# Kernel tuning notes

Hardware: AMD Instinct MI355X
Metric: run time of the kernel (lower is better)

The kernel has to match this reference:

```python
import jax, jax.numpy as jnp
import numpy as np

V, C, H, L, FC, OUT, WS = 512, 256, 4, 6, 1024, 192, 4
HD = C // H
B, T = 8, 1024


def setup_inputs() -> dict:
    key = jax.random.key(0)
    ks = jax.random.split(key, 24)
    d = {}
    d['emb'] = jax.random.normal(ks[0], (V, C), jnp.float32) * C ** -0.5
    d['Wq'] = jax.random.normal(ks[1], (L, C, C), jnp.float32) * 0.02
    d['Wk'] = jax.random.normal(ks[2], (L, C, C), jnp.float32) * 0.02
    d['Wv'] = jax.random.normal(ks[3], (L, C, C), jnp.float32) * 0.02
    d['Wo'] = jax.random.normal(ks[4], (L, C, C), jnp.float32) * 0.02
    d['bq'] = jnp.zeros((L, C), jnp.float32)
    d['bk'] = jnp.zeros((L, C), jnp.float32)
    d['bv'] = jnp.zeros((L, C), jnp.float32)
    d['bo'] = jnp.zeros((L, C), jnp.float32)
    d['rel_k'] = jax.random.normal(ks[5], (L, 2 * WS + 1, HD), jnp.float32) * HD ** -0.5
    d['rel_v'] = jax.random.normal(ks[6], (L, 2 * WS + 1, HD), jnp.float32) * HD ** -0.5
    d['ln1_g'] = jnp.ones((L, C), jnp.float32)
    d['ln1_b'] = jnp.zeros((L, C), jnp.float32)
    d['ln2_g'] = jnp.ones((L, C), jnp.float32)
    d['ln2_b'] = jnp.zeros((L, C), jnp.float32)
    d['ffn_w1'] = jax.random.normal(ks[7], (L, C, FC), jnp.float32) * 0.02
    d['ffn_b1'] = jnp.zeros((L, FC), jnp.float32)
    d['ffn_w2'] = jax.random.normal(ks[8], (L, FC, C), jnp.float32) * 0.02
    d['ffn_b2'] = jnp.zeros((L, C), jnp.float32)
    d['proj_w'] = jax.random.normal(ks[9], (2 * OUT, C), jnp.float32) * 0.02
    d['proj_b'] = jnp.zeros((2 * OUT,), jnp.float32)
    d['tokens'] = jax.random.randint(ks[10], (B, T), 0, V)
    d['x_lengths'] = jax.random.randint(ks[11], (B,), T // 2, T + 1)
    return d


def _rel_to_abs(x):
    # x: [B,H,L,2L-1] -> [B,H,L,L]
    b, h, l, _ = x.shape
    x = jnp.pad(x, ((0, 0), (0, 0), (0, 0), (0, 1)))
    x = x.reshape(b, h, l * 2 * l)
    x = jnp.pad(x, ((0, 0), (0, 0), (0, l - 1)))
    x = x.reshape(b, h, l + 1, 2 * l - 1)
    return x[:, :, :l, l - 1:]


def _abs_to_rel(x):
    # x: [B,H,L,L] -> [B,H,L,2L-1]
    b, h, l, _ = x.shape
    x = jnp.pad(x, ((0, 0), (0, 0), (0, 0), (0, l - 1)))
    x = x.reshape(b, h, l * (2 * l - 1))
    x = jnp.pad(x, ((0, 0), (0, 0), (l, 0)))
    x = x.reshape(b, h, l, 2 * l)
    return x[:, :, :, 1:]


def _layernorm(x, g, b):
    m = jnp.mean(x, -1, keepdims=True)
    v = jnp.var(x, -1, keepdims=True)
    return (x - m) * jax.lax.rsqrt(v + 1e-5) * g + b


def _pad_rel(emb, t):
    # [2*WS+1, HD] -> [2t-1, HD] (t > WS+1 here)
    p = t - (WS + 1)
    return jnp.pad(emb, ((p, p), (0, 0)))


def _forward(emb, Wq, Wk, Wv, Wo, bq, bk, bv, bo, rel_k, rel_v, ln1_g, ln1_b,
             ln2_g, ln2_b, ffn_w1, ffn_b1, ffn_w2, ffn_b2, proj_w, proj_b,
             tokens, x_lengths):
    b, t = tokens.shape
    x = emb[tokens] * jnp.sqrt(jnp.float32(C))          # [B,T,C]
    mask = (jnp.arange(t)[None, :] < x_lengths[:, None]).astype(x.dtype)  # [B,T]
    attn_mask = mask[:, None, None, :] * mask[:, None, :, None]           # [B,1,T,T]

    for i in range(L):
        q = (x @ Wq[i] + bq[i]).reshape(b, t, H, HD).transpose(0, 2, 1, 3)
        k = (x @ Wk[i] + bk[i]).reshape(b, t, H, HD).transpose(0, 2, 1, 3)
        v = (x @ Wv[i] + bv[i]).reshape(b, t, H, HD).transpose(0, 2, 1, 3)
        q = q * HD ** -0.5
        scores = jnp.einsum('bhqd,bhkd->bhqk', q, k)
        rk = _pad_rel(rel_k[i], t)                      # [2T-1,HD]
        scores = scores + _rel_to_abs(jnp.einsum('bhqd,md->bhqm', q, rk))
        scores = jnp.where(attn_mask > 0, scores, -1e4)
        p = jax.nn.softmax(scores, axis=-1)             # [B,H,T,T]
        o = jnp.einsum('bhqk,bhkd->bhqd', p, v)
        rv = _pad_rel(rel_v[i], t)
        o = o + jnp.einsum('bhqm,md->bhqd', _abs_to_rel(p), rv)
        o = o.transpose(0, 2, 1, 3).reshape(b, t, C) @ Wo[i] + bo[i]
        x = _layernorm(x + o, ln1_g[i], ln1_b[i])
        f = jax.nn.relu(x @ ffn_w1[i] + ffn_b1[i]) @ ffn_w2[i] + ffn_b2[i]
        x = _layernorm(x + f, ln2_g[i], ln2_b[i])
        x = x * mask[:, :, None]

    x_bct = x.transpose(0, 2, 1)                        # [B,C,T]
    stats = (jnp.einsum('oc,bct->bot', proj_w, x_bct) + proj_b[None, :, None])
    stats = stats * mask[:, None, :]
    m, logs = stats[:, :OUT], stats[:, OUT:]
    return x_bct, m, logs, mask[:, None, :]


def reference(emb, Wq, Wk, Wv, Wo, bq, bk, bv, bo, rel_k, rel_v, ln1_g, ln1_b,
              ln2_g, ln2_b, ffn_w1, ffn_b1, ffn_w2, ffn_b2, proj_w, proj_b,
              tokens, x_lengths):
    return _forward(emb, Wq, Wk, Wv, Wo, bq, bk, bv, bo, rel_k, rel_v, ln1_g,
                    ln1_b, ln2_g, ln2_b, ffn_w1, ffn_b1, ffn_w2, ffn_b2,
                    proj_w, proj_b, tokens, x_lengths)
```

## Files before the change

### kernel.cpp

```cpp
#include <hip/hip_runtime.h>

typedef unsigned short u16;
typedef __attribute__((ext_vector_type(8))) short bf16x8;
typedef __attribute__((ext_vector_type(4))) float f32x4;

#define CC   256
#define HH   4
#define HD   64
#define LL   6
#define FCD  1024
#define OUTD 192
#define WSZ  4
#define BB   8
#define TT   1024
#define BT   8192

#define OFF_XBCT 0
#define OFF_M    2097152
#define OFF_LOGS 3670016
#define OFF_MASK 5242880

#define WT_Q   0
#define WT_K   65536
#define WT_V   131072
#define WT_O   196608
#define WT_W1  262144
#define WT_W2  524288
#define WT_LAYER 786432
#define WT_TOTAL (6 * WT_LAYER)

__device__ __forceinline__ float bf2f(u16 u) {
  union { unsigned int i; float f; } v; v.i = ((unsigned int)u) << 16; return v.f;
}
__device__ __forceinline__ u16 f2bf(float f) {
  union { float f; unsigned int i; } v; v.f = f;
  unsigned int x = v.i;
  return (u16)((x + 0x7fffu + ((x >> 16) & 1u)) >> 16);
}
__device__ __forceinline__ void ldv4(const float* p, float* o) {
  float4 v = *reinterpret_cast<const float4*>(p);
  o[0] = v.x; o[1] = v.y; o[2] = v.z; o[3] = v.w;
}
__device__ __forceinline__ float ld_e(const float* p) { return *p; }
__device__ __forceinline__ float ld_e(const u16* p)   { return bf2f(*p); }
__device__ __forceinline__ void st_e(float* p, float v) { *p = v; }
__device__ __forceinline__ void st_e(u16* p, float v)   { *p = f2bf(v); }

__device__ __forceinline__ void gload16(const u16* g, u16* l) {
  __builtin_amdgcn_global_load_lds(
      (const __attribute__((address_space(1))) unsigned int*)g,
      (__attribute__((address_space(3))) unsigned int*)l, 16, 0, 0);
}

__device__ __forceinline__ void stage8(const float* p, u16* d) {
  float4 a = *reinterpret_cast<const float4*>(p);
  float4 b = *reinterpret_cast<const float4*>(p + 4);
  d[0] = f2bf(a.x); d[1] = f2bf(a.y); d[2] = f2bf(a.z); d[3] = f2bf(a.w);
  d[4] = f2bf(b.x); d[5] = f2bf(b.y); d[6] = f2bf(b.z); d[7] = f2bf(b.w);
}
__device__ __forceinline__ void stage8(const u16* p, u16* d) {
  ushort4 a = *reinterpret_cast<const ushort4*>(p);
  ushort4 b = *reinterpret_cast<const ushort4*>(p + 4);
  d[0] = a.x; d[1] = a.y; d[2] = a.z; d[3] = a.w;
  d[4] = b.x; d[5] = b.y; d[6] = b.z; d[7] = b.w;
}

__global__ __launch_bounds__(256) void tc_k(
    const float* __restrict__ W, u16* __restrict__ WT,
    int K, int N, int dstStride)
{
  __shared__ float tl[32][33];
  const int tid = threadIdx.x;
  const int lx = tid & 31;
  const int ly = tid >> 5;
  const int n0 = blockIdx.x << 5;
  const int k0 = blockIdx.y << 5;
  const int z  = blockIdx.z;
  const float* Ws = W + (size_t)z * K * N;
  u16* WTd = WT + (size_t)z * dstStride;
#pragma unroll
  for (int r = 0; r < 4; ++r)
    tl[ly + r * 8][lx] = Ws[(size_t)(k0 + ly + r * 8) * N + (n0 + lx)];
  __syncthreads();
#pragma unroll
  for (int r = 0; r < 4; ++r)
    WTd[(size_t)(n0 + ly + r * 8) * K + (k0 + lx)] = f2bf(tl[lx][ly + r * 8]);
}

__global__ __launch_bounds__(256) void embed_k(
    const float* __restrict__ emb, const int* __restrict__ tokens,
    float* __restrict__ X, u16* __restrict__ Xb)
{
  const int i = blockIdx.x * 256 + threadIdx.x;
  const int bt = i >> 6;
  const int c  = (i & 63) << 2;
  float4 e = *reinterpret_cast<const float4*>(emb + (size_t)tokens[bt] * CC + c);
  e.x *= 16.0f; e.y *= 16.0f; e.z *= 16.0f; e.w *= 16.0f;
  *reinterpret_cast<float4*>(X + (size_t)i * 4) = e;
  if (Xb)
    *reinterpret_cast<ushort4*>(Xb + (size_t)i * 4) =
        make_ushort4(f2bf(e.x), f2bf(e.y), f2bf(e.z), f2bf(e.w));
}

template <typename CT>
__global__ __launch_bounds__(256) void gemm_t_k(
    const u16* __restrict__ A, int lda, const u16* __restrict__ B, int ldb,
    const float* __restrict__ bias, CT* __restrict__ C, int ldc,
    int K, float ps, int relu, int accum)
{
  __shared__ __align__(16) u16 As[64 * 64];
  __shared__ __align__(16) u16 Bs[64 * 64];
  const int tid  = threadIdx.x;
  const int lane = tid & 63;
  const int wv   = tid >> 6;
  const int bm = blockIdx.y * 64;
  const int bn = blockIdx.x * 64;
  const int l15 = lane & 15;
  const int lq  = lane >> 4;
  const int sb0 = wv << 10;
  const int sb1 = sb0 + 512;
  const int r0  = (wv << 4) + (lane >> 3);
  const int r1  = r0 + 8;
  const int sc  = ((lane & 7) ^ (lane >> 3)) << 3;
  const int asw = (l15 & 7) << 3;

  f32x4 acc[4];
#pragma unroll
  for (int nt = 0; nt < 4; ++nt) acc[nt] = (f32x4){0.0f, 0.0f, 0.0f, 0.0f};

  for (int k0 = 0; k0 < K; k0 += 64) {
    gload16(A + (size_t)(bm + r0) * lda + (k0 + sc), As + sb0);
    gload16(A + (size_t)(bm + r1) * lda + (k0 + sc), As + sb1);
    gload16(B + (size_t)(bn + r0) * ldb + (k0 + sc), Bs + sb0);
    gload16(B + (size_t)(bn + r1) * ldb + (k0 + sc), Bs + sb1);
    __syncthreads();
#pragma unroll
    for (int s = 0; s < 2; ++s) {
      const int cbase = (s << 5) | (lq << 3);
      const bf16x8 af = *reinterpret_cast<const bf16x8*>(
          As + (((wv << 4) + l15) << 6) + (cbase ^ asw));
#pragma unroll
      for (int nt = 0; nt < 4; ++nt) {
        const bf16x8 bf = *reinterpret_cast<const bf16x8*>(
            Bs + (((nt << 4) + l15) << 6) + (cbase ^ asw));
        acc[nt] = __builtin_amdgcn_mfma_f32_16x16x32_bf16(af, bf, acc[nt], 0, 0, 0);
      }
    }
    __syncthreads();
  }

#pragma unroll
  for (int nt = 0; nt < 4; ++nt) {
#pragma unroll
    for (int r = 0; r < 4; ++r) {
      const int row = bm + (wv << 4) + (lq << 2) + r;
      const int col = bn + (nt << 4) + l15;
      float vv = acc[nt][r];
      if (bias) vv += bias[col];
      vv *= ps;
      if (relu) vv = fmaxf(vv, 0.0f);
      const size_t ci = (size_t)row * ldc + col;
      if (accum) vv += ld_e(C + ci);
      st_e(C + ci, vv);
    }
  }
}

__global__ __launch_bounds__(256) void gemm_ln_k(
    const u16* __restrict__ A, int lda, const u16* __restrict__ B, int ldb,
    const float* __restrict__ bias,
    float* __restrict__ X, u16* __restrict__ Xb,
    const float* __restrict__ g, const float* __restrict__ be,
    const int* __restrict__ xlen, int am, int K)
{
  __shared__ __align__(16) u16 As[16 * 64];
  __shared__ __align__(16) u16 Bs[256 * 64];
  __shared__ float part[16][4];
  __shared__ float part2[16][4];
  const int tid  = threadIdx.x;
  const int lane = tid & 63;
  const int wv   = tid >> 6;
  const int bm   = blockIdx.x << 4;
  const int l15  = lane & 15;
  const int lq   = lane >> 4;
  const int sc   = ((lane & 7) ^ (lane >> 3)) << 3;
  const int asw  = (l15 & 7) << 3;

  f32x4 acc[4];
#pragma unroll
  for (int nt = 0; nt < 4; ++nt) acc[nt] = (f32x4){0.0f, 0.0f, 0.0f, 0.0f};

  for (int k0 = 0; k0 < K; k0 += 64) {
    if (wv < 2)
      gload16(A + (size_t)(bm + (wv << 3) + (lane >> 3)) * lda + (k0 + sc),
              As + (wv << 9));
#pragma unroll
    for (int j = 0; j < 8; ++j)
      gload16(B + (size_t)((wv << 6) + (j << 3) + (lane >> 3)) * ldb + (k0 + sc),
              Bs + (wv << 12) + (j << 9));
    __syncthreads();
#pragma unroll
    for (int s = 0; s < 2; ++s) {
      const int cbase = (s << 5) | (lq << 3);
      const bf16x8 af = *reinterpret_cast<const bf16x8*>(
          As + (l15 << 6) + (cbase ^ asw));
#pragma unroll
      for (int nt = 0; nt < 4; ++nt) {
        const bf16x8 bf = *reinterpret_cast<const bf16x8*>(
            Bs + (((wv << 6) + (nt << 4) + l15) << 6) + (cbase ^ asw));
        acc[nt] = __builtin_amdgcn_mfma_f32_16x16x32_bf16(af, bf, acc[nt], 0, 0, 0);
      }
    }
    __syncthreads();
  }

  float v[4][4];
#pragma unroll
  for (int nt = 0; nt < 4; ++nt) {
    const int col = (wv << 6) + (nt << 4) + l15;
#pragma unroll
    for (int reg = 0; reg < 4; ++reg) {
      const int gr = bm + (lq << 2) + reg;
      v[nt][reg] = acc[nt][reg] + bias[col] + X[(size_t)gr * CC + col];
    }
  }
  float sr[4];
#pragma unroll
  for (int reg = 0; reg < 4; ++reg) {
    float s = v[0][reg] + v[1][reg] + v[2][reg] + v[3][reg];
    s += __shfl_xor(s, 1); s += __shfl_xor(s, 2);
    s += __shfl_xor(s, 4); s += __shfl_xor(s, 8);
    sr[reg] = s;
  }
  if (l15 == 0) {
#pragma unroll
    for (int reg = 0; reg < 4; ++reg) part[(lq << 2) + reg][wv] = sr[reg];
  }
  __syncthreads();
  float mean[4];
#pragma unroll
  for (int reg = 0; reg < 4; ++reg) {
    const int r = (lq << 2) + reg;
    mean[reg] = (part[r][0] + part[r][1] + part[r][2] + part[r][3]) * (1.0f / CC);
  }
#pragma unroll
  for (int reg = 0; reg < 4; ++reg) {
    float s2 = 0.0f;
#pragma unroll
    for (int nt = 0; nt < 4; ++nt) {
      v[nt][reg] -= mean[reg];
      s2 += v[nt][reg] * v[nt][reg];
    }
    s2 += __shfl_xor(s2, 1); s2 += __shfl_xor(s2, 2);
    s2 += __shfl_xor(s2, 4); s2 += __shfl_xor(s2, 8);
    sr[reg] = s2;
  }
  if (l15 == 0) {
#pragma unroll
    for (int reg = 0; reg < 4; ++reg) part2[(lq << 2) + reg][wv] = sr[reg];
  }
  __syncthreads();
#pragma unroll
  for (int reg = 0; reg < 4; ++reg) {
    const int r = (lq << 2) + reg;
    const int gr = bm + r;
    const int b = gr >> 10;
    const int t = gr & (TT - 1);
    const float var = (part2[r][0] + part2[r][1] + part2[r][2] + part2[r][3]) * (1.0f / CC);
    const float rs = rsqrtf(var + 1e-5f);
    const bool zero = (am && t >= xlen[b]);
#pragma unroll
    for (int nt = 0; nt < 4; ++nt) {
      const int col = (wv << 6) + (nt << 4) + l15;
      float y = v[nt][reg] * rs * g[col] + be[col];
      if (zero) y = 0.0f;
      X[(size_t)gr * CC + col] = y;
      Xb[(size_t)gr * CC + col] = f2bf(y);
    }
  }
}

__global__ __launch_bounds__(256) void gemm_qkv_k(
    const u16* __restrict__ Xb, const u16* __restrict__ WTl,
    const float* __restrict__ bq, const float* __restrict__ bk,
    const float* __restrict__ bv,
    u16* __restrict__ Qb, u16* __restrict__ Kb, u16* __restrict__ Vb)
{
  __shared__ __align__(16) u16 pool[2 * 64 * 64];
  u16* As = pool;
  u16* Bs = pool + 4096;
  const int tid  = threadIdx.x;
  const int lane = tid & 63;
  const int wv   = tid >> 6;
  const int bx = blockIdx.x;
  const int bm = blockIdx.y * 64;
  const int mi = bx >> 2;
  const int bnl = (bx & 3) << 6;
  const int bng = bx << 6;
  const int l15 = lane & 15;
  const int lq  = lane >> 4;
  const int sb0 = wv << 10;
  const int sb1 = sb0 + 512;
  const int r0  = (wv << 4) + (lane >> 3);
  const int r1  = r0 + 8;
  const int sc  = ((lane & 7) ^ (lane >> 3)) << 3;
  const int asw = (l15 & 7) << 3;

  const float* bias = (mi == 0) ? bq : (mi == 1) ? bk : bv;
  const float ps = (mi == 0) ? 0.125f : 1.0f;

  f32x4 acc[4];
#pragma unroll
  for (int nt = 0; nt < 4; ++nt) acc[nt] = (f32x4){0.0f, 0.0f, 0.0f, 0.0f};

  for (int k0 = 0; k0 < CC; k0 += 64) {
    gload16(Xb  + (size_t)(bm + r0) * CC + (k0 + sc), As + sb0);
    gload16(Xb  + (size_t)(bm + r1) * CC + (k0 + sc), As + sb1);
    gload16(WTl + (size_t)(bng + r0) * CC + (k0 + sc), Bs + sb0);
    gload16(WTl + (size_t)(bng + r1) * CC + (k0 + sc), Bs + sb1);
    __syncthreads();
#pragma unroll
    for (int s = 0; s < 2; ++s) {
      const int cbase = (s << 5) | (lq << 3);
      const bf16x8 af = *reinterpret_cast<const bf16x8*>(
          As + (((wv << 4) + l15) << 6) + (cbase ^ asw));
#pragma unroll
      for (int nt = 0; nt < 4; ++nt) {
        const bf16x8 bf = *reinterpret_cast<const bf16x8*>(
            Bs + (((nt << 4) + l15) << 6) + (cbase ^ asw));
        acc[nt] = __builtin_amdgcn_mfma_f32_16x16x32_bf16(af, bf, acc[nt], 0, 0, 0);
      }
    }
    __syncthreads();
  }

  if (mi != 2) {
    u16* Cp = (mi == 0) ? Qb : Kb;
#pragma unroll
    for (int nt = 0; nt < 4; ++nt) {
#pragma unroll
      for (int r = 0; r < 4; ++r) {
        const int row = bm + (wv << 4) + (lq << 2) + r;
        const int col = bnl + (nt << 4) + l15;
        Cp[(size_t)row * CC + col] = f2bf((acc[nt][r] + bias[col]) * ps);
      }
    }
  } else {
    u16* Ts = pool;
#pragma unroll
    for (int nt = 0; nt < 4; ++nt) {
#pragma unroll
      for (int r = 0; r < 4; ++r) {
        const int tl = (wv << 4) + (lq << 2) + r;
        const int dl = (nt << 4) + l15;
        Ts[dl * 72 + tl] = f2bf(acc[nt][r] + bias[bnl + dl]);
      }
    }
    __syncthreads();
    const int dl = tid >> 2;
    const size_t rowbase =
        ((size_t)((bm >> 10) * 256 + bnl + dl) << 10) + (bm & (TT - 1));
#pragma unroll
    for (int j = 0; j < 4; ++j) {
      const int c4 = ((tid & 3) << 2) + (j << 4);
      *reinterpret_cast<ushort4*>(Vb + rowbase + c4) =
          *reinterpret_cast<const ushort4*>(Ts + dl * 72 + c4);
    }
  }
}

template <typename AT, typename CT>
__global__ __launch_bounds__(256) void gemm_m_k(
    const AT* __restrict__ A, const float* __restrict__ W, int ldb,
    const float* __restrict__ bias, CT* __restrict__ C, int ldc,
    int K, float ps, int relu, int accum, int vtrans)
{
  __shared__ u16 As[64][40];
  __shared__ u16 Bs[64][40];
  const int tid  = threadIdx.x;
  const int lane = tid & 63;
  const int wv   = tid >> 6;
  const int bm = blockIdx.y * 64;
  const int bn = blockIdx.x * 64;
  const int l15 = lane & 15;
  const int lq  = lane >> 4;
  const int ar = tid >> 2;
  const int ak = (tid & 3) << 3;
  const int kr = tid & 31;
  const int nb = (tid >> 5) << 3;

  f32x4 acc[4];
#pragma unroll
  for (int nt = 0; nt < 4; ++nt) acc[nt] = (f32x4){0.0f, 0.0f, 0.0f, 0.0f};

  for (int k0 = 0; k0 < K; k0 += 32) {
    u16 t8[8];
    stage8(A + (size_t)(bm + ar) * K + (k0 + ak), t8);
    *reinterpret_cast<ushort4*>(&As[ar][ak]) =
        make_ushort4(t8[0], t8[1], t8[2], t8[3]);
    *reinterpret_cast<ushort4*>(&As[ar][ak + 4]) =
        make_ushort4(t8[4], t8[5], t8[6], t8[7]);
    float w8[8];
    ldv4(W + (size_t)(k0 + kr) * ldb + (bn + nb), w8);
    ldv4(W + (size_t)(k0 + kr) * ldb + (bn + nb + 4), w8 + 4);
#pragma unroll
    for (int j = 0; j < 8; ++j) Bs[nb + j][kr] = f2bf(w8[j]);
    __syncthreads();

    const bf16x8 af = *reinterpret_cast<const bf16x8*>(&As[(wv << 4) + l15][lq << 3]);
#pragma unroll
    for (int nt = 0; nt < 4; ++nt) {
      const bf16x8 bf = *reinterpret_cast<const bf16x8*>(&Bs[(nt << 4) + l15][lq << 3]);
      acc[nt] = __builtin_amdgcn_mfma_f32_16x16x32_bf16(af, bf, acc[nt], 0, 0, 0);
    }
    __syncthreads();
  }

#pragma unroll
  for (int nt = 0; nt < 4; ++nt) {
#pragma unroll
    for (int r = 0; r < 4; ++r) {
      const int row = bm + (wv << 4) + (lq << 2) + r;
      const int col = bn + (nt << 4) + l15;
      float vv = acc[nt][r];
      if (bias) vv += bias[col];
      vv *= ps;
      if (relu) vv = fmaxf(vv, 0.0f);
      if (vtrans) {
        const size_t dst = ((size_t)((row >> 10) * 256 + col) << 10) + (row & (TT - 1));
        st_e(C + dst, vv);
      } else {
        const size_t ci = (size_t)row * ldc + col;
        if (accum) vv += ld_e(C + ci);
        st_e(C + ci, vv);
      }
    }
  }
}

#define KLp(g) (KVpool + (g) * 4096)
#define VTp(g) (KVpool + 8192 + (g) * 4096)
__global__ __launch_bounds__(512, 4) void fattn_k(
    const u16* __restrict__ Qb, const u16* __restrict__ Kb,
    const u16* __restrict__ VbT, const float* __restrict__ rk,
    const float* __restrict__ rv, const int* __restrict__ xlen,
    u16* __restrict__ Ob)
{
  __shared__ __align__(16) u16 KVpool[4 * 64 * 64];
  __shared__ u16  Pl[2][64][64];
  __shared__ float rkl[9][64];
  __shared__ float rvl[9][68];
  __shared__ float qrel[64][12];
  __shared__ float bs_s[64][12];
  __shared__ float mrow_s[64];

  const int qt = blockIdx.x;
  const int bh = blockIdx.y;
  const int b  = bh >> 2;
  const int h  = bh & 3;
  const int tid  = threadIdx.x;
  const int lane = tid & 63;
  const int wv   = tid >> 6;
  const int grp  = wv >> 2;
  const int wvl  = wv & 3;
  const int gtid = tid & 255;
  const int l15  = lane & 15;
  const int lq   = lane >> 4;
  const int len = xlen[b];
  const int q0  = qt << 6;
  const int m0  = wvl << 4;

  if (q0 >= len) {
    for (int i = tid; i < 64 * 16; i += 512) {
      const int r = i >> 4, c4 = (i & 15) << 2;
      *reinterpret_cast<ushort4*>(
          Ob + (size_t)((b << 10) + q0 + r) * CC + (h << 6) + c4) =
          make_ushort4(0, 0, 0, 0);
    }
    return;
  }

  for (int i = tid; i < 9 * 64; i += 512) {
    rkl[i >> 6][i & 63] = rk[i];
    rvl[i >> 6][i & 63] = rv[i];
  }
  for (int i = tid; i < 64 * 16; i += 512) {
    const int r = i >> 4, c4 = (i & 15) << 2;
    *reinterpret_cast<ushort4*>(&Pl[0][r][c4]) = *reinterpret_cast<const ushort4*>(
        Qb + (size_t)((b << 10) + q0 + r) * CC + (h << 6) + c4);
  }
  for (int i = tid; i < 64 * 12; i += 512) (&bs_s[0][0])[i] = -3.0e38f;
  __syncthreads();
  for (int i = tid; i < 64 * 9; i += 512) {
    const int r = i / 9, j = i - r * 9;
    float s = 0.0f;
#pragma unroll 16
    for (int d = 0; d < 64; ++d) s += bf2f(Pl[0][r][d]) * rkl[j][d];
    qrel[r][j] = s;
  }
  __syncthreads();

  const bf16x8 qa0 = *reinterpret_cast<const bf16x8*>(&Pl[0][m0 + l15][lq << 3]);
  const bf16x8 qa1 = *reinterpret_cast<const bf16x8*>(&Pl[0][m0 + l15][32 + (lq << 3)]);

  f32x4 oacc[4];
#pragma unroll
  for (int nt = 0; nt < 4; ++nt) oacc[nt] = (f32x4){0.0f, 0.0f, 0.0f, 0.0f};
  float m_r[4] = {-3.0e38f, -3.0e38f, -3.0e38f, -3.0e38f};
  float l_r[4] = {0.0f, 0.0f, 0.0f, 0.0f};

  const int gr = gtid >> 2;
  const int gc = (gtid & 3) << 4;
  const int rswG = (gr & 7) << 3;
  const int c0w = gc ^ rswG;
  const int c1w = (gc + 8) ^ rswG;
  const int rswF = (l15 & 7) << 3;

  const int nkt = (len + 63) >> 6;
  const int nt0 = (nkt + 1) >> 1;
  const int myBeg = grp ? nt0 : 0;
  const int myEnd = grp ? nkt : nt0;

  u16* klp = KLp(grp);
  u16* vtp = VTp(grp);
  u16* plp = &Pl[grp][0][0];

  bf16x8 kp0, kp1, vq0, vq1;
  if (myBeg < myEnd) {
    const int k0 = myBeg << 6;
    const u16* p = Kb + (size_t)((b << 10) + k0 + gr) * CC + (h << 6) + gc;
    kp0 = *reinterpret_cast<const bf16x8*>(p);
    kp1 = *reinterpret_cast<const bf16x8*>(p + 8);
    const u16* pv = VbT + (size_t)((bh << 6) + gr) * TT + k0 + gc;
    vq0 = *reinterpret_cast<const bf16x8*>(pv);
    vq1 = *reinterpret_cast<const bf16x8*>(pv + 8);
  }

  for (int it = 0; it < nt0; ++it) {
    const int kt = myBeg + it;
    const bool act = (kt < myEnd);
    if (act) {
      *reinterpret_cast<bf16x8*>(klp + gr * 64 + c0w) = kp0;
      *reinterpret_cast<bf16x8*>(klp + gr * 64 + c1w) = kp1;
      *reinterpret_cast<bf16x8*>(vtp + gr * 64 + c0w) = vq0;
      *reinterpret_cast<bf16x8*>(vtp + gr * 64 + c1w) = vq1;
    }
    __syncthreads();

    if (act && kt + 1 < myEnd) {
      const int kn = (kt + 1) << 6;
      const u16* p = Kb + (size_t)((b << 10) + kn + gr) * CC + (h << 6) + gc;
      kp0 = *reinterpret_cast<const bf16x8*>(p);
      kp1 = *reinterpret_cast<const bf16x8*>(p + 8);
      const u16* pv = VbT + (size_t)((bh << 6) + gr) * TT + kn + gc;
      vq0 = *reinterpret_cast<const bf16x8*>(pv);
      vq1 = *reinterpret_cast<const bf16x8*>(pv + 8);
    }

    if (act) {
      const int k0 = kt << 6;
      f32x4 sacc[4];
#pragma unroll
      for (int nt = 0; nt < 4; ++nt) sacc[nt] = (f32x4){0.0f, 0.0f, 0.0f, 0.0f};
#pragma unroll
      for (int nt = 0; nt < 4; ++nt) {
        const int row = (nt << 4) + l15;
        const bf16x8 b0 = *reinterpret_cast<const bf16x8*>(klp + row * 64 + ((lq << 3) ^ rswF));
        const bf16x8 b1 = *reinterpret_cast<const bf16x8*>(klp + row * 64 + ((32 + (lq << 3)) ^ rswF));
        sacc[nt] = __builtin_amdgcn_mfma_f32_16x16x32_bf16(qa0, b0, sacc[nt], 0, 0, 0);
        sacc[nt] = __builtin_amdgcn_mfma_f32_16x16x32_bf16(qa1, b1, sacc[nt], 0, 0, 0);
      }
#pragma unroll
      for (int nt = 0; nt < 4; ++nt) {
#pragma unroll
        for (int reg = 0; reg < 4; ++reg) {
          const int m = m0 + (lq << 2) + reg;
          const int q = q0 + m;
          const int k = k0 + (nt << 4) + l15;
          float s = sacc[nt][reg];
          const int r = k - q;
          const bool band = (r >= -WSZ && r <= WSZ);
          if (band) s += qrel[m][r + WSZ];
          if (q >= len || k >= len) s = -10000.0f;
          if (band) bs_s[m][r + WSZ] = s;
          sacc[nt][reg] = s;
        }
      }
      float aa[4];
#pragma unroll
      for (int reg = 0; reg < 4; ++reg) {
        float mx = fmaxf(fmaxf(sacc[0][reg], sacc[1][reg]),
                         fmaxf(sacc[2][reg], sacc[3][reg]));
        mx = fmaxf(mx, __shfl_xor(mx, 1));
        mx = fmaxf(mx, __shfl_xor(mx, 2));
        mx = fmaxf(mx, __shfl_xor(mx, 4));
        mx = fmaxf(mx, __shfl_xor(mx, 8));
        const float mo = m_r[reg];
        const float mn = fmaxf(mo, mx);
        const float a = __expf(mo - mn);
        m_r[reg] = mn; aa[reg] = a; l_r[reg] *= a;
      }
#pragma unroll
      for (int reg = 0; reg < 4; ++reg) {
        const int m = m0 + (lq << 2) + reg;
        const int msw = (m & 7) << 3;
        const float mn = m_r[reg];
        float ssum = 0.0f;
#pragma unroll
        for (int nt = 0; nt < 4; ++nt) {
          const float p = __expf(sacc[nt][reg] - mn);
          ssum += p;
          plp[m * 64 + (((nt << 4) + l15) ^ msw)] = f2bf(p);
        }
        ssum += __shfl_xor(ssum, 1);
        ssum += __shfl_xor(ssum, 2);
        ssum += __shfl_xor(ssum, 4);
        ssum += __shfl_xor(ssum, 8);
        l_r[reg] += ssum;
      }
#pragma unroll
      for (int nt = 0; nt < 4; ++nt) {
#pragma unroll
        for (int reg = 0; reg < 4; ++reg) oacc[nt][reg] *= aa[reg];
      }
      {
        const int prow = m0 + l15;
        const bf16x8 p0 = *reinterpret_cast<const bf16x8*>(plp + prow * 64 + ((lq << 3) ^ rswF));
        const bf16x8 p1 = *reinterpret_cast<const bf16x8*>(plp + prow * 64 + ((32 + (lq << 3)) ^ rswF));
#pragma unroll
        for (int nt = 0; nt < 4; ++nt) {
          const int row = (nt << 4) + l15;
          const bf16x8 v0 = *reinterpret_cast<const bf16x8*>(vtp + row * 64 + ((lq << 3) ^ rswF));
          const bf16x8 v1 = *reinterpret_cast<const bf16x8*>(vtp + row * 64 + ((32 + (lq << 3)) ^ rswF));
          oacc[nt] = __builtin_amdgcn_mfma_f32_16x16x32_bf16(p0, v0, oacc[nt], 0, 0, 0);
          oacc[nt] = __builtin_amdgcn_mfma_f32_16x16x32_bf16(p1, v1, oacc[nt], 0, 0, 0);
        }
      }
    }
    __syncthreads();
  }

  float* Oc = (float*)KVpool;
  float* mxp = Oc + 64 * 68;
  float* lxp = mxp + 64;
  if (grp == 1) {
#pragma unroll
    for (int nt = 0; nt < 4; ++nt)
#pragma unroll
      for (int reg = 0; reg < 4; ++reg)
        Oc[(m0 + (lq << 2) + reg) * 68 + (nt << 4) + l15] = oacc[nt][reg];
    if (l15 == 0) {
#pragma unroll
      for (int reg = 0; reg < 4; ++reg) {
        mxp[m0 + (lq << 2) + reg] = m_r[reg];
        lxp[m0 + (lq << 2) + reg] = l_r[reg];
      }
    }
  }
  __syncthreads();
  if (grp == 0) {
    float a0c[4], a1c[4];
#pragma unroll
    for (int reg = 0; reg < 4; ++reg) {
      const int m = m0 + (lq << 2) + reg;
      const float m1 = mxp[m], l1 = lxp[m];
      const float mo = m_r[reg];
      const float mn = fmaxf(mo, m1);
      const float a0 = __expf(mo - mn);
      const float a1 = __expf(m1 - mn);
      m_r[reg] = mn;
      l_r[reg] = a0 * l_r[reg] + a1 * l1;
      a0c[reg] = a0; a1c[reg] = a1;
    }
#pragma unroll
    for (int nt = 0; nt < 4; ++nt)
#pragma unroll
      for (int reg = 0; reg < 4; ++reg) {
        const int m = m0 + (lq << 2) + reg;
        oacc[nt][reg] = a0c[reg] * oacc[nt][reg]
                      + a1c[reg] * Oc[m * 68 + (nt << 4) + l15];
      }
    if (l15 == 0) {
#pragma unroll
      for (int reg = 0; reg < 4; ++reg)
        mrow_s[m0 + (lq << 2) + reg] = m_r[reg];
    }
  }
  __syncthreads();
  for (int i = tid; i < 64 * 9; i += 512) {
    const int r = i / 9, j = i - r * 9;
    qrel[r][j] = __expf(bs_s[r][j] - mrow_s[r]);
  }
  __syncthreads();
  if (grp == 0) {
#pragma unroll
    for (int nt = 0; nt < 4; ++nt) {
#pragma unroll
      for (int reg = 0; reg < 4; ++reg) {
        const int m = m0 + (lq << 2) + reg;
        float o = oacc[nt][reg];
#pragma unroll
        for (int j = 0; j < 9; ++j) o += qrel[m][j] * rvl[j][(nt << 4) + l15];
        o *= 1.0f / l_r[reg];
        Ob[(size_t)((b << 10) + q0 + m) * CC + (h << 6) + (nt << 4) + l15] = f2bf(o);
      }
    }
  }
}

__global__ __launch_bounds__(256) void addln_k(
    float* __restrict__ X, u16* __restrict__ Xb, const float* __restrict__ R,
    const float* __restrict__ g, const float* __restrict__ be,
    const int* __restrict__ xlen, int am)
{
  const int tid = threadIdx.x;
  const int row = blockIdx.x * 4 + (tid >> 6);
  const int lane = tid & 63;
  const int b = row >> 10;
  const int t = row & (TT - 1);
  const size_t base = (size_t)row * CC + lane * 4;
  float4 xv = *reinterpret_cast<const float4*>(X + base);
  float4 rv = *reinterpret_cast<const float4*>(R + base);
  float v0 = xv.x + rv.x, v1 = xv.y + rv.y, v2 = xv.z + rv.z, v3 = xv.w + rv.w;
  float s = v0 + v1 + v2 + v3;
#pragma unroll
  for (int off = 32; off > 0; off >>= 1) s += __shfl_xor(s, off);
  const float mean = s * (1.0f / CC);
  const float d0 = v0 - mean, d1 = v1 - mean, d2 = v2 - mean, d3 = v3 - mean;
  float s2 = d0 * d0 + d1 * d1 + d2 * d2 + d3 * d3;
#pragma unroll
  for (int off = 32; off > 0; off >>= 1) s2 += __shfl_xor(s2, off);
  const float rs = rsqrtf(s2 * (1.0f / CC) + 1e-5f);
  const float4 gv = *reinterpret_cast<const float4*>(g + lane * 4);
  const float4 bv = *reinterpret_cast<const float4*>(be + lane * 4);
  float y0 = d0 * rs * gv.x + bv.x;
  float y1 = d1 * rs * gv.y + bv.y;
  float y2 = d2 * rs * gv.z + bv.z;
  float y3 = d3 * rs * gv.w + bv.w;
  if (am && t >= xlen[b]) { y0 = 0.0f; y1 = 0.0f; y2 = 0.0f; y3 = 0.0f; }
  *reinterpret_cast<float4*>(X + base) = make_float4(y0, y1, y2, y3);
  if (Xb)
    *reinterpret_cast<ushort4*>(Xb + base) =
        make_ushort4(f2bf(y0), f2bf(y1), f2bf(y2), f2bf(y3));
}

__global__ __launch_bounds__(256) void proj_k(
    const float* __restrict__ A, const float* __restrict__ W,
    const float* __restrict__ bias, const int* __restrict__ xlen,
    float* __restrict__ out)
{
  __shared__ u16 As[64][40];
  __shared__ u16 Bs[64][40];
  const int tid  = threadIdx.x;
  const int lane = tid & 63;
  const int wv   = tid >> 6;
  const int bm = blockIdx.y * 64;
  const int bn = blockIdx.x * 64;
  const int l15 = lane & 15;
  const int lq  = lane >> 4;
  const int ar = tid >> 2;
  const int ak = (tid & 3) << 3;

  f32x4 acc[4];
#pragma unroll
  for (int nt = 0; nt < 4; ++nt) acc[nt] = (f32x4){0.0f, 0.0f, 0.0f, 0.0f};

  for (int k0 = 0; k0 < CC; k0 += 32) {
    u16 t8[8];
    stage8(A + (size_t)(bm + ar) * CC + (k0 + ak), t8);
    *reinterpret_cast<ushort4*>(&As[ar][ak]) =
        make_ushort4(t8[0], t8[1], t8[2], t8[3]);
    *reinterpret_cast<ushort4*>(&As[ar][ak + 4]) =
        make_ushort4(t8[4], t8[5], t8[6], t8[7]);
    stage8(W + (size_t)(bn + ar) * CC + (k0 + ak), t8);
    *reinterpret_cast<ushort4*>(&Bs[ar][ak]) =
        make_ushort4(t8[0], t8[1], t8[2], t8[3]);
    *reinterpret_cast<ushort4*>(&Bs[ar][ak + 4]) =
        make_ushort4(t8[4], t8[5], t8[6], t8[7]);
    __syncthreads();

    const bf16x8 af = *reinterpret_cast<const bf16x8*>(&As[(wv << 4) + l15][lq << 3]);
#pragma unroll
    for (int nt = 0; nt < 4; ++nt) {
      const bf16x8 bf = *reinterpret_cast<const bf16x8*>(&Bs[(nt << 4) + l15][lq << 3]);
      acc[nt] = __builtin_amdgcn_mfma_f32_16x16x32_bf16(af, bf, acc[nt], 0, 0, 0);
    }
    __syncthreads();
  }

#pragma unroll
  for (int nt = 0; nt < 4; ++nt) {
#pragma unroll
    for (int r = 0; r < 4; ++r) {
      const int row = bm + (wv << 4) + (lq << 2) + r;
      const int bb = row >> 10;
      const int t  = row & (TT - 1);
      const int len = xlen[bb];
      const int o = bn + (nt << 4) + l15;
      float vv = acc[nt][r] + bias[o];
      if (t >= len) vv = 0.0f;
      const size_t dst = (o < OUTD)
          ? (size_t)OFF_M    + ((size_t)bb * OUTD + o) * TT + t
          : (size_t)OFF_LOGS + ((size_t)bb * OUTD + (o - OUTD)) * TT + t;
      out[dst] = vv;
    }
  }
}

__global__ __launch_bounds__(256) void pack_xbct_k(
    const float* __restrict__ X, float* __restrict__ out)
{
  __shared__ float tl[32][33];
  const int tid = threadIdx.x;
  const int lx = tid & 31;
  const int ly = tid >> 5;
  const int c0 = blockIdx.x << 5;
  const int t0 = blockIdx.y << 5;
  const int b  = blockIdx.z;
#pragma unroll
  for (int r = 0; r < 4; ++r)
    tl[ly + r * 8][lx] = X[(((size_t)(b << 10) + t0 + ly + r * 8) << 8) + c0 + lx];
  __syncthreads();
#pragma unroll
  for (int r = 0; r < 4; ++r)
    out[OFF_XBCT + (((size_t)b * 256 + c0 + ly + r * 8) << 10) + t0 + lx] =
        tl[lx][ly + r * 8];
}

__global__ __launch_bounds__(256) void pack_mask_k(
    const int* __restrict__ xlen, float* __restrict__ out)
{
  const int i = blockIdx.x * 256 + threadIdx.x;
  const int b = i >> 10;
  const int t = i & (TT - 1);
  out[OFF_MASK + i] = (t < xlen[b]) ? 1.0f : 0.0f;
}

extern "C" void kernel_launch(void* const* d_in, const int* in_sizes, int n_in,
                              void* d_out, int out_size, void* d_ws, size_t ws_size,
                              hipStream_t stream)
{
  (void)in_sizes; (void)n_in; (void)out_size;
  const float* emb   = (const float*)d_in[0];
  const float* Wq    = (const float*)d_in[1];
  const float* Wk    = (const float*)d_in[2];
  const float* Wv    = (const float*)d_in[3];
  const float* Wo    = (const float*)d_in[4];
  const float* bq    = (const float*)d_in[5];
  const float* bk    = (const float*)d_in[6];
  const float* bv    = (const float*)d_in[7];
  const float* bo    = (const float*)d_in[8];
  const float* relk  = (const float*)d_in[9];
  const float* relv  = (const float*)d_in[10];
  const float* ln1g  = (const float*)d_in[11];
  const float* ln1b  = (const float*)d_in[12];
  const float* ln2g  = (const float*)d_in[13];
  const float* ln2b  = (const float*)d_in[14];
  const float* W1    = (const float*)d_in[15];
  const float* b1    = (const float*)d_in[16];
  const float* W2    = (const float*)d_in[17];
  const float* b2    = (const float*)d_in[18];
  const float* projw = (const float*)d_in[19];
  const float* projb = (const float*)d_in[20];
  const int*   tokens = (const int*)d_in[21];
  const int*   xlen   = (const int*)d_in[22];
  float* out = (float*)d_out;

  const size_t TIER_B_WS = 26214400ull;
  const size_t TIER_A_WS = 38797312ull;
  const int tier = (ws_size >= TIER_A_WS) ? 0 : (ws_size >= TIER_B_WS) ? 1 : 2;

  float* X  = (float*)d_ws;
  u16* ObU = (u16*)(out + OFF_XBCT);
  u16* Kb  = (u16*)(out + OFF_M);
  u16* Vb  = (u16*)(out + OFF_LOGS);
  float* T5 = out + OFF_M;

  if (tier <= 1) {
    u16* Xb  = (u16*)(X + (size_t)BT * CC);
    u16* Wbf = Xb + (size_t)BT * CC;
    u16* pool = Wbf + WT_TOTAL;
    u16* Qb = pool;
    u16* Hc = pool;
    const int CH = (tier == 0) ? 1 : 4;
    const int Wn = FCD / CH;

    tc_k<<<dim3(8, 8, 6), 256, 0, stream>>>(Wq, Wbf + WT_Q, CC, CC, WT_LAYER);
    tc_k<<<dim3(8, 8, 6), 256, 0, stream>>>(Wk, Wbf + WT_K, CC, CC, WT_LAYER);
    tc_k<<<dim3(8, 8, 6), 256, 0, stream>>>(Wv, Wbf + WT_V, CC, CC, WT_LAYER);
    tc_k<<<dim3(8, 8, 6), 256, 0, stream>>>(Wo, Wbf + WT_O, CC, CC, WT_LAYER);
    tc_k<<<dim3(32, 8, 6), 256, 0, stream>>>(W1, Wbf + WT_W1, CC, FCD, WT_LAYER);
    tc_k<<<dim3(8, 32, 6), 256, 0, stream>>>(W2, Wbf + WT_W2, FCD, CC, WT_LAYER);

    embed_k<<<(BT * CC / 4) / 256, 256, 0, stream>>>(emb, tokens, X, Xb);

    const dim3 gQKV(12, BT / 64);
    const dim3 gA(16, BB * HH);
    const dim3 gP((2 * OUTD) / 64, BT / 64);

    for (int l = 0; l < LL; ++l) {
      const u16* WTl = Wbf + (size_t)l * WT_LAYER;
      gemm_qkv_k<<<gQKV, 256, 0, stream>>>(Xb, WTl, bq + (size_t)l * CC,
                                           bk + (size_t)l * CC, bv + (size_t)l * CC,
                                           Qb, Kb, Vb);
      fattn_k<<<gA, 512, 0, stream>>>(Qb, Kb, Vb,
                                      relk + (size_t)l * (2 * WSZ + 1) * HD,
                                      relv + (size_t)l * (2 * WSZ + 1) * HD, xlen, ObU);
      gemm_ln_k<<<BT / 16, 256, 0, stream>>>(ObU, CC, WTl + WT_O, CC,
                                             bo + (size_t)l * CC, X, Xb,
                                             ln1g + (size_t)l * CC,
                                             ln1b + (size_t)l * CC, xlen, 0, CC);
      if (CH == 1) {
        gemm_t_k<u16><<<dim3(FCD / 64, BT / 64), 256, 0, stream>>>(
            Xb, CC, WTl + WT_W1, CC, b1 + (size_t)l * FCD, Hc, FCD, CC,
            1.0f, 1, 0);
        gemm_ln_k<<<BT / 16, 256, 0, stream>>>(Hc, FCD, WTl + WT_W2, FCD,
                                               b2 + (size_t)l * CC, X, Xb,
                                               ln2g + (size_t)l * CC,
                                               ln2b + (size_t)l * CC, xlen, 1, FCD);
      } else {
        const dim3 gC(CC / 64, BT / 64);
        for (int c = 0; c < CH; ++c) {
          gemm_t_k<u16><<<dim3(Wn / 64, BT / 64), 256, 0, stream>>>(
              Xb, CC, WTl + WT_W1 + (size_t)c * Wn * CC, CC,
              b1 + (size_t)l * FCD + c * Wn, Hc, Wn, CC, 1.0f, 1, 0);
          gemm_t_k<float><<<gC, 256, 0, stream>>>(
              Hc, Wn, WTl + WT_W2 + (size_t)c * Wn, FCD,
              (c == 0) ? (b2 + (size_t)l * CC) : nullptr, T5, CC, Wn,
              1.0f, 0, (c > 0));
        }
        addln_k<<<BT / 4, 256, 0, stream>>>(X, Xb, T5, ln2g + (size_t)l * CC,
                                            ln2b + (size_t)l * CC, xlen, 1);
      }
    }

    proj_k<<<gP, 256, 0, stream>>>(X, projw, projb, xlen, out);
  } else {
    u16* pool = (u16*)(X + (size_t)BT * CC);
    u16* Qb = pool;
    u16* Hc = pool;

    embed_k<<<(BT * CC / 4) / 256, 256, 0, stream>>>(emb, tokens, X, nullptr);

    const dim3 gC(CC / 64, BT / 64);
    const dim3 gA(16, BB * HH);
    const dim3 gP((2 * OUTD) / 64, BT / 64);

    for (int l = 0; l < LL; ++l) {
      const float* Wq_l = Wq + (size_t)l * CC * CC;
      const float* Wk_l = Wk + (size_t)l * CC * CC;
      const float* Wv_l = Wv + (size_t)l * CC * CC;
      const float* Wo_l = Wo + (size_t)l * CC * CC;

      gemm_m_k<float, u16><<<gC, 256, 0, stream>>>(X, Wq_l, CC, bq + (size_t)l * CC,
                                                   Qb, CC, CC, 0.125f, 0, 0, 0);
      gemm_m_k<float, u16><<<gC, 256, 0, stream>>>(X, Wk_l, CC, bk + (size_t)l * CC,
                                                   Kb, CC, CC, 1.0f, 0, 0, 0);
      gemm_m_k<float, u16><<<gC, 256, 0, stream>>>(X, Wv_l, CC, bv + (size_t)l * CC,
                                                   Vb, CC, CC, 1.0f, 0, 0, 1);
      fattn_k<<<gA, 512, 0, stream>>>(Qb, Kb, Vb,
                                      relk + (size_t)l * (2 * WSZ + 1) * HD,
                                      relv + (size_t)l * (2 * WSZ + 1) * HD, xlen, ObU);
      gemm_m_k<u16, float><<<gC, 256, 0, stream>>>(ObU, Wo_l, CC, bo + (size_t)l * CC,
                                                   T5, CC, CC, 1.0f, 0, 0, 0);
      addln_k<<<BT / 4, 256, 0, stream>>>(X, nullptr, T5, ln1g + (size_t)l * CC,
                                          ln1b + (size_t)l * CC, xlen, 0);
      for (int c = 0; c < 4; ++c) {
        gemm_m_k<float, u16><<<gC, 256, 0, stream>>>(X, W1 + (size_t)l * CC * FCD + c * 256,
                                                     FCD, b1 + (size_t)l * FCD + c * 256,
                                                     Hc, 256, CC, 1.0f, 1, 0, 0);
        gemm_m_k<u16, float><<<gC, 256, 0, stream>>>(Hc,
                                                     W2 + (size_t)l * FCD * CC + (size_t)c * 256 * CC,
                                                     CC, (c == 0) ? (b2 + (size_t)l * CC) : nullptr,
                                                     T5, CC, 256, 1.0f, 0, (c > 0), 0);
      }
      addln_k<<<BT / 4, 256, 0, stream>>>(X, nullptr, T5, ln2g + (size_t)l * CC,
                                          ln2b + (size_t)l * CC, xlen, 1);
    }

    proj_k<<<gP, 256, 0, stream>>>(X, projw, projb, xlen, out);
  }

  pack_xbct_k<<<dim3(CC / 32, TT / 32, BB), 256, 0, stream>>>(X, out);
  pack_mask_k<<<(BB * TT) / 256, 256, 0, stream>>>(xlen, out);
}
```

Baseline: 692.6 us.

## Use 128x128-tile GEMM for FFN up-projection and raise MFMA priority in attention

Adds a gemm128_k kernel in which each wave computes a 64x64 sub-tile (4x4 MFMA fragments) of a 128x128 block, and uses it for the FFN W1 GEMM with ReLU in place of the 64x64-tile gemm_t_k. The larger tile reuses each A and B fragment loaded from LDS across more MFMAs, cutting LDS and global traffic per flop. The trade is more registers and only 512 blocks for the GEMM. It also wraps the MFMA sequences in the attention kernel with s_setprio(1)/s_setprio(0) so waves issuing matrix work are favored by the scheduler. gemm_ln_k is moved below gemm128_k unchanged, and the unused stage16 helper is added.

```diff
diff --git a/kernel.cpp b/kernel.cpp
--- a/kernel.cpp
+++ b/kernel.cpp
@@ -63,6 +63,10 @@
   ushort4 b = *reinterpret_cast<const ushort4*>(p + 4);
   d[0] = a.x; d[1] = a.y; d[2] = a.z; d[3] = a.w;
   d[4] = b.x; d[5] = b.y; d[6] = b.z; d[7] = b.w;
+}
+__device__ __forceinline__ void stage16(const u16* src, u16* dst) {
+  *reinterpret_cast<bf16x8*>(dst)     = *reinterpret_cast<const bf16x8*>(src);
+  *reinterpret_cast<bf16x8*>(dst + 8) = *reinterpret_cast<const bf16x8*>(src + 8);
 }
 
 __global__ __launch_bounds__(256) void tc_k(
@@ -166,116 +170,77 @@
   }
 }
 
-__global__ __launch_bounds__(256) void gemm_ln_k(
+template <typename CT>
+__global__ __launch_bounds__(256) void gemm128_k(
     const u16* __restrict__ A, int lda, const u16* __restrict__ B, int ldb,
-    const float* __restrict__ bias,
-    float* __restrict__ X, u16* __restrict__ Xb,
-    const float* __restrict__ g, const float* __restrict__ be,
-    const int* __restrict__ xlen, int am, int K)
-{
-  __shared__ __align__(16) u16 As[16 * 64];
-  __shared__ __align__(16) u16 Bs[256 * 64];
-  __shared__ float part[16][4];
-  __shared__ float part2[16][4];
+    const float* __restrict__ bias, CT* __restrict__ C, int ldc,
+    int K, float ps, int relu)
+{
+  __shared__ __align__(16) u16 As[128 * 64];
+  __shared__ __align__(16) u16 Bs[128 * 64];
   const int tid  = threadIdx.x;
   const int lane = tid & 63;
   const int wv   = tid >> 6;
-  const int bm   = blockIdx.x << 4;
-  const int l15  = lane & 15;
-  const int lq   = lane >> 4;
-  const int sc   = ((lane & 7) ^ (lane >> 3)) << 3;
-  const int asw  = (l15 & 7) << 3;
-
-  f32x4 acc[4];
-#pragma unroll
-  for (int nt = 0; nt < 4; ++nt) acc[nt] = (f32x4){0.0f, 0.0f, 0.0f, 0.0f};
+  const int bm = blockIdx.y * 128;
+  const int bn = blockIdx.x * 128;
+  const int l15 = lane & 15;
+  const int lq  = lane >> 4;
+  const int wr  = (wv >> 1) << 6;
+  const int wc  = (wv & 1) << 6;
+  const int rbase = wv << 5;
+  const int rlane = lane >> 3;
+  const int sc  = ((lane & 7) ^ rlane) << 3;
+  const int asw = (l15 & 7) << 3;
+
+  f32x4 acc[4][4];
+#pragma unroll
+  for (int mf = 0; mf < 4; ++mf)
+#pragma unroll
+    for (int nf = 0; nf < 4; ++nf) acc[mf][nf] = (f32x4){0.0f, 0.0f, 0.0f, 0.0f};
 
   for (int k0 = 0; k0 < K; k0 += 64) {
-    if (wv < 2)
-      gload16(A + (size_t)(bm + (wv << 3) + (lane >> 3)) * lda + (k0 + sc),
-              As + (wv << 9));
-#pragma unroll
-    for (int j = 0; j < 8; ++j)
-      gload16(B + (size_t)((wv << 6) + (j << 3) + (lane >> 3)) * ldb + (k0 + sc),
-              Bs + (wv << 12) + (j << 9));
+#pragma unroll
+    for (int j = 0; j < 4; ++j) {
+      gload16(A + (size_t)(bm + rbase + (j << 3) + rlane) * lda + (k0 + sc),
+              As + ((rbase + (j << 3)) << 6));
+      gload16(B + (size_t)(bn + rbase + (j << 3) + rlane) * ldb + (k0 + sc),
+              Bs + ((rbase + (j << 3)) << 6));
+    }
     __syncthreads();
 #pragma unroll
     for (int s = 0; s < 2; ++s) {
-      const int cbase = (s << 5) | (lq << 3);
-      const bf16x8 af = *reinterpret_cast<const bf16x8*>(
-          As + (l15 << 6) + (cbase ^ asw));
-#pragma unroll
-      for (int nt = 0; nt < 4; ++nt) {
+      const int cb = ((s << 5) | (lq << 3)) ^ asw;
+      bf16x8 af[4];
+#pragma unroll
+      for (int mf = 0; mf < 4; ++mf)
+        af[mf] = *reinterpret_cast<const bf16x8*>(
+            As + ((wr + (mf << 4) + l15) << 6) + cb);
+#pragma unroll
+      for (int nf = 0; nf < 4; ++nf) {
         const bf16x8 bf = *reinterpret_cast<const bf16x8*>(
-            Bs + (((wv << 6) + (nt << 4) + l15) << 6) + (cbase ^ asw));
-        acc[nt] = __builtin_amdgcn_mfma_f32_16x16x32_bf16(af, bf, acc[nt], 0, 0, 0);
-      }
-    }
-    __syncthreads();
-  }
-
-  float v[4][4];
-#pragma unroll
-  for (int nt = 0; nt < 4; ++nt) {
-    const int col = (wv << 6) + (nt << 4) + l15;
-#pragma unroll
-    for (int reg = 0; reg < 4; ++reg) {
-      const int gr = bm + (lq << 2) + reg;
-      v[nt][reg] = acc[nt][reg] + bias[col] + X[(size_t)gr * CC + col];
-    }
-  }
-  float sr[4];
-#pragma unroll
-  for (int reg = 0; reg < 4; ++reg) {
-    float s = v[0][reg] + v[1][reg] + v[2][reg] + v[3][reg];
-    s += __shfl_xor(s, 1); s += __shfl_xor(s, 2);
-    s += __shfl_xor(s, 4); s += __shfl_xor(s, 8);
-    sr[reg] = s;
-  }
-  if (l15 == 0) {
-#pragma unroll
-    for (int reg = 0; reg < 4; ++reg) part[(lq << 2) + reg][wv] = sr[reg];
-  }
-  __syncthreads();
-  float mean[4];
-#pragma unroll
-  for (int reg = 0; reg < 4; ++reg) {
-    const int r = (lq << 2) + reg;
-    mean[reg] = (part[r][0] + part[r][1] + part[r][2] + part[r][3]) * (1.0f / CC);
-  }
-#pragma unroll
-  for (int reg = 0; reg < 4; ++reg) {
-    float s2 = 0.0f;
-#pragma unroll
-    for (int nt = 0; nt < 4; ++nt) {
-      v[nt][reg] -= mean[reg];
-      s2 += v[nt][reg] * v[nt][reg];
-    }
-    s2 += __shfl_xor(s2, 1); s2 += __shfl_xor(s2, 2);
-    s2 += __shfl_xor(s2, 4); s2 += __shfl_xor(s2, 8);
-    sr[reg] = s2;
-  }
-  if (l15 == 0) {
-#pragma unroll
-    for (int reg = 0; reg < 4; ++reg) part2[(lq << 2) + reg][wv] = sr[reg];
-  }
-  __syncthreads();
-#pragma unroll
-  for (int reg = 0; reg < 4; ++reg) {
-    const int r = (lq << 2) + reg;
-    const int gr = bm + r;
-    const int b = gr >> 10;
-    const int t = gr & (TT - 1);
-    const float var = (part2[r][0] + part2[r][1] + part2[r][2] + part2[r][3]) * (1.0f / CC);
-    const float rs = rsqrtf(var + 1e-5f);
-    const bool zero = (am && t >= xlen[b]);
-#pragma unroll
-    for (int nt = 0; nt < 4; ++nt) {
-      const int col = (wv << 6) + (nt << 4) + l15;
-      float y = v[nt][reg] * rs * g[col] + be[col];
-      if (zero) y = 0.0f;
-      X[(size_t)gr * CC + col] = y;
-      Xb[(size_t)gr * CC + col] = f2bf(y);
+            Bs + ((wc + (nf << 4) + l15) << 6) + cb);
+#pragma unroll
+        for (int mf = 0; mf < 4; ++mf)
+          acc[mf][nf] = __builtin_amdgcn_mfma_f32_16x16x32_bf16(af[mf], bf, acc[mf][nf], 0, 0, 0);
+      }
+    }
+    __syncthreads();
+  }
+
+#pragma unroll
+  for (int mf = 0; mf < 4; ++mf) {
+#pragma unroll
+    for (int nf = 0; nf < 4; ++nf) {
+#pragma unroll
+      for (int reg = 0; reg < 4; ++reg) {
+        const int row = bm + wr + (mf << 4) + (lq << 2) + reg;
+        const int col = bn + wc + (nf << 4) + l15;
+        float vv = acc[mf][nf][reg];
+        if (bias) vv += bias[col];
+        vv *= ps;
+        if (relu) vv = fmaxf(vv, 0.0f);
+        st_e(C + (size_t)row * ldc + col, vv);
+      }
     }
   }
 }
@@ -369,6 +334,120 @@
   }
 }
 
+__global__ __launch_bounds__(256) void gemm_ln_k(
+    const u16* __restrict__ A, int lda, const u16* __restrict__ B, int ldb,
+    const float* __restrict__ bias,
+    float* __restrict__ X, u16* __restrict__ Xb,
+    const float* __restrict__ g, const float* __restrict__ be,
+    const int* __restrict__ xlen, int am, int K)
+{
+  __shared__ __align__(16) u16 As[16 * 64];
+  __shared__ __align__(16) u16 Bs[256 * 64];
+  __shared__ float part[16][4];
+  __shared__ float part2[16][4];
+  const int tid  = threadIdx.x;
+  const int lane = tid & 63;
+  const int wv   = tid >> 6;
+  const int bm   = blockIdx.x << 4;
+  const int l15  = lane & 15;
+  const int lq   = lane >> 4;
+  const int sc   = ((lane & 7) ^ (lane >> 3)) << 3;
+  const int asw  = (l15 & 7) << 3;
+
+  f32x4 acc[4];
+#pragma unroll
+  for (int nt = 0; nt < 4; ++nt) acc[nt] = (f32x4){0.0f, 0.0f, 0.0f, 0.0f};
+
+  for (int k0 = 0; k0 < K; k0 += 64) {
+    if (wv < 2)
+      gload16(A + (size_t)(bm + (wv << 3) + (lane >> 3)) * lda + (k0 + sc),
+              As + (wv << 9));
+#pragma unroll
+    for (int j = 0; j < 8; ++j)
+      gload16(B + (size_t)((wv << 6) + (j << 3) + (lane >> 3)) * ldb + (k0 + sc),
+              Bs + (wv << 12) + (j << 9));
+    __syncthreads();
+#pragma unroll
+    for (int s = 0; s < 2; ++s) {
+      const int cbase = (s << 5) | (lq << 3);
+      const bf16x8 af = *reinterpret_cast<const bf16x8*>(
+          As + (l15 << 6) + (cbase ^ asw));
+#pragma unroll
+      for (int nt = 0; nt < 4; ++nt) {
+        const bf16x8 bf = *reinterpret_cast<const bf16x8*>(
+            Bs + (((wv << 6) + (nt << 4) + l15) << 6) + (cbase ^ asw));
+        acc[nt] = __builtin_amdgcn_mfma_f32_16x16x32_bf16(af, bf, acc[nt], 0, 0, 0);
+      }
+    }
+    __syncthreads();
+  }
+
+  float v[4][4];
+#pragma unroll
+  for (int nt = 0; nt < 4; ++nt) {
+    const int col = (wv << 6) + (nt << 4) + l15;
+#pragma unroll
+    for (int reg = 0; reg < 4; ++reg) {
+      const int gr = bm + (lq << 2) + reg;
+      v[nt][reg] = acc[nt][reg] + bias[col] + X[(size_t)gr * CC + col];
+    }
+  }
+  float sr[4];
+#pragma unroll
+  for (int reg = 0; reg < 4; ++reg) {
+    float s = v[0][reg] + v[1][reg] + v[2][reg] + v[3][reg];
+    s += __shfl_xor(s, 1); s += __shfl_xor(s, 2);
+    s += __shfl_xor(s, 4); s += __shfl_xor(s, 8);
+    sr[reg] = s;
+  }
+  if (l15 == 0) {
+#pragma unroll
+    for (int reg = 0; reg < 4; ++reg) part[(lq << 2) + reg][wv] = sr[reg];
+  }
+  __syncthreads();
+  float mean[4];
+#pragma unroll
+  for (int reg = 0; reg < 4; ++reg) {
+    const int r = (lq << 2) + reg;
+    mean[reg] = (part[r][0] + part[r][1] + part[r][2] + part[r][3]) * (1.0f / CC);
+  }
+#pragma unroll
+  for (int reg = 0; reg < 4; ++reg) {
+    float s2 = 0.0f;
+#pragma unroll
+    for (int nt = 0; nt < 4; ++nt) {
+      v[nt][reg] -= mean[reg];
+      s2 += v[nt][reg] * v[nt][reg];
+    }
+    s2 += __shfl_xor(s2, 1); s2 += __shfl_xor(s2, 2);
+    s2 += __shfl_xor(s2, 4); s2 += __shfl_xor(s2, 8);
+    sr[reg] = s2;
+  }
+  if (l15 == 0) {
+#pragma unroll
+    for (int reg = 0; reg < 4; ++reg) part2[(lq << 2) + reg][wv] = sr[reg];
+  }
+  __syncthreads();
+#pragma unroll
+  for (int reg = 0; reg < 4; ++reg) {
+    const int r = (lq << 2) + reg;
+    const int gr = bm + r;
+    const int b = gr >> 10;
+    const int t = gr & (TT - 1);
+    const float var = (part2[r][0] + part2[r][1] + part2[r][2] + part2[r][3]) * (1.0f / CC);
+    const float rs = rsqrtf(var + 1e-5f);
+    const bool zero = (am && t >= xlen[b]);
+#pragma unroll
+    for (int nt = 0; nt < 4; ++nt) {
+      const int col = (wv << 6) + (nt << 4) + l15;
+      float y = v[nt][reg] * rs * g[col] + be[col];
+      if (zero) y = 0.0f;
+      X[(size_t)gr * CC + col] = y;
+      Xb[(size_t)gr * CC + col] = f2bf(y);
+    }
+  }
+}
+
 template <typename AT, typename CT>
 __global__ __launch_bounds__(256) void gemm_m_k(
     const AT* __restrict__ A, const float* __restrict__ W, int ldb,
@@ -562,6 +641,7 @@
       f32x4 sacc[4];
 #pragma unroll
       for (int nt = 0; nt < 4; ++nt) sacc[nt] = (f32x4){0.0f, 0.0f, 0.0f, 0.0f};
+      __builtin_amdgcn_s_setprio(1);
 #pragma unroll
       for (int nt = 0; nt < 4; ++nt) {
         const int row = (nt << 4) + l15;
@@ -570,6 +650,7 @@
         sacc[nt] = __builtin_amdgcn_mfma_f32_16x16x32_bf16(qa0, b0, sacc[nt], 0, 0, 0);
         sacc[nt] = __builtin_amdgcn_mfma_f32_16x16x32_bf16(qa1, b1, sacc[nt], 0, 0, 0);
       }
+      __builtin_amdgcn_s_setprio(0);
 #pragma unroll
       for (int nt = 0; nt < 4; ++nt) {
 #pragma unroll
@@ -627,6 +708,7 @@
         const int prow = m0 + l15;
         const bf16x8 p0 = *reinterpret_cast<const bf16x8*>(plp + prow * 64 + ((lq << 3) ^ rswF));
         const bf16x8 p1 = *reinterpret_cast<const bf16x8*>(plp + prow * 64 + ((32 + (lq << 3)) ^ rswF));
+        __builtin_amdgcn_s_setprio(1);
 #pragma unroll
         for (int nt = 0; nt < 4; ++nt) {
           const int row = (nt << 4) + l15;
@@ -635,6 +717,7 @@
           oacc[nt] = __builtin_amdgcn_mfma_f32_16x16x32_bf16(p0, v0, oacc[nt], 0, 0, 0);
           oacc[nt] = __builtin_amdgcn_mfma_f32_16x16x32_bf16(p1, v1, oacc[nt], 0, 0, 0);
         }
+        __builtin_amdgcn_s_setprio(0);
       }
     }
     __syncthreads();
@@ -911,9 +994,9 @@
                                              ln1g + (size_t)l * CC,
                                              ln1b + (size_t)l * CC, xlen, 0, CC);
       if (CH == 1) {
-        gemm_t_k<u16><<<dim3(FCD / 64, BT / 64), 256, 0, stream>>>(
+        gemm128_k<u16><<<dim3(FCD / 128, BT / 128), 256, 0, stream>>>(
             Xb, CC, WTl + WT_W1, CC, b1 + (size_t)l * FCD, Hc, FCD, CC,
-            1.0f, 1, 0);
+            1.0f, 1);
         gemm_ln_k<<<BT / 16, 256, 0, stream>>>(Hc, FCD, WTl + WT_W2, FCD,
                                                b2 + (size_t)l * CC, X, Xb,
                                                ln2g + (size_t)l * CC,
```

Result: slower. 727.4 us (+5.0%).
